# Optimization experiments

Measured on AMD Instinct MI355X. Metric: run time of the kernel, lower is better.

The kernel has to match this reference:

```python
import jax, jax.numpy as jnp
import numpy as np

P = 16           # patch size
D = 768          # embed / feature dim (= 3*P*P)
T = 8            # number of task vectors
H_META = 192     # MetaNet hidden (= D // 4)


def patchify(x):
    # x: [B, 3, H, W] -> [B, N, 3*P*P]
    B, C, H, W = x.shape
    x = x.reshape(B, C, H // P, P, W // P, P)
    x = x.transpose(0, 2, 4, 1, 3, 5)
    return x.reshape(B, (H // P) * (W // P), C * P * P)


def encode(W1, b1, W2, b2, x):
    # base functional encoder f(params, x): shared weights over the batch
    patches = patchify(x)                       # [B, N, D]
    h = jax.nn.relu(patches @ W1 + b1)          # [B, N, D]
    pooled = h.mean(axis=1)                     # [B, D]
    return pooled @ W2 + b2                     # [B, D]


def setup_inputs() -> dict:
    key = jax.random.key(0)
    ks = jax.random.split(key, 14)
    B = 64
    s = 0.02
    return {
        "x":   jax.random.normal(ks[0], (B, 3, 224, 224), jnp.float32),
        # base model params
        "W1":  jax.random.normal(ks[1], (D, D), jnp.float32) * s,
        "b1":  jax.random.normal(ks[2], (D,), jnp.float32) * s,
        "W2":  jax.random.normal(ks[3], (D, D), jnp.float32) * s,
        "b2":  jax.random.normal(ks[4], (D,), jnp.float32) * s,
        # task-vector deltas (stacked over T tasks)
        "dW1": jax.random.normal(ks[5], (T, D, D), jnp.float32) * s,
        "db1": jax.random.normal(ks[6], (T, D), jnp.float32) * s,
        "dW2": jax.random.normal(ks[7], (T, D, D), jnp.float32) * s,
        "db2": jax.random.normal(ks[8], (T, D), jnp.float32) * s,
        # MetaNet (Linear-ReLU-Linear); zero-init in the original, random here
        "mw1": jax.random.normal(ks[9], (D, H_META), jnp.float32) * s,
        "mb1": jax.random.normal(ks[10], (H_META,), jnp.float32) * s,
        "mw2": jax.random.normal(ks[11], (H_META, T), jnp.float32) * s,
        "mb2": jax.random.normal(ks[12], (T,), jnp.float32) * s,
    }


def reference(x, W1, b1, W2, b2, dW1, db1, dW2, db2, mw1, mb1, mw2, mb2):
    # 1) base features with frozen base model (torch.no_grad)
    base = jax.lax.stop_gradient(encode(W1, b1, W2, b2, x))       # [B, D]
    # 2) per-sample mixing coefficients via MetaNet
    coefs = jax.nn.relu(base @ mw1 + mb1) @ mw2 + mb2             # [B, T]
    # 3) per-sample mixed parameters: p + sum_t c[b,t] * dp[t]
    nW1 = W1 + jnp.einsum("bt,tij->bij", coefs, dW1)              # [B, D, D]
    nb1 = b1 + coefs @ db1                                        # [B, D]
    nW2 = W2 + jnp.einsum("bt,tij->bij", coefs, dW2)              # [B, D, D]
    nb2 = b2 + coefs @ db2                                        # [B, D]
    # 4) batched per-sample forward with the mixed weights
    patches = patchify(x)                                         # [B, N, D]
    h = jax.nn.relu(jnp.einsum("bnd,bde->bne", patches, nW1) + nb1[:, None, :])
    pooled = h.mean(axis=1)                                       # [B, D]
    out = jnp.einsum("bd,bde->be", pooled, nW2) + nb2             # [B, D]
    return out
```

## Files before the change

### kernel.cpp

```cpp
#include <hip/hip_runtime.h>
#include <hip/hip_bf16.h>


typedef __bf16 bf16x8 __attribute__((ext_vector_type(8)));
typedef float f32x4 __attribute__((ext_vector_type(4)));
typedef __hip_bfloat16 bf16;

struct alignas(16) BF8 { bf16 h[8]; };

constexpr int BATCH = 64;
constexpr int NP    = 196;
constexpr int NPAD  = 256;
constexpr int DIM   = 768;
constexpr int NT    = 8;
constexpr size_t MSZ = (size_t)DIM * DIM;

__device__ __forceinline__ void async_cp16(const void* g, void* l) {
  __builtin_amdgcn_global_load_lds(
      (const __attribute__((address_space(1))) uint32_t*)g,
      (__attribute__((address_space(3))) uint32_t*)l, 16, 0, 0);
}

constexpr int PREP_PATCH_BLOCKS = (BATCH * NPAD * (DIM / 4)) / 256;
constexpr int PREP_TRANS_BLOCKS = 24 * 24 * 18;

__global__ void k_prep(const float* __restrict__ x, bf16* __restrict__ A,
                       const float* __restrict__ W1, const float* __restrict__ dW1,
                       const float* __restrict__ W2, const float* __restrict__ dW2,
                       bf16* __restrict__ WT) {
  __shared__ float tile[32][33];
  int blk = blockIdx.x;
  int tid = threadIdx.x;
  if (blk < PREP_PATCH_BLOCKS) {
    int idx  = blk * 256 + tid;
    int col4 = idx % (DIM / 4);
    int row  = idx / (DIM / 4);
    int d = col4 * 4;
    int b = row >> 8;
    int n = row & 255;
    bf16 tmp[4];
    if (n < NP) {
      int hp = n / 14, wp = n % 14;
      int c  = d >> 8;
      int rr = d & 255;
      int i = rr >> 4, j = rr & 15;
      const float* src = x + ((((size_t)b * 3 + c) * 224 + hp * 16 + i) * 224 + wp * 16 + j);
      float4 f = *(const float4*)src;
      tmp[0] = __float2bfloat16(f.x);
      tmp[1] = __float2bfloat16(f.y);
      tmp[2] = __float2bfloat16(f.z);
      tmp[3] = __float2bfloat16(f.w);
    } else {
      tmp[0] = tmp[1] = tmp[2] = tmp[3] = __float2bfloat16(0.0f);
    }
    *(ushort4*)(A + (size_t)row * DIM + d) = *(ushort4*)tmp;
  } else {
    int tb  = blk - PREP_PATCH_BLOCKS;
    int mat = tb / 576;
    int rem = tb % 576;
    int n0 = (rem % 24) * 32;
    int k0 = (rem / 24) * 32;
    const float* src;
    if      (mat == 0) src = W1;
    else if (mat <= 8) src = dW1 + (size_t)(mat - 1) * MSZ;
    else if (mat == 9) src = W2;
    else               src = dW2 + (size_t)(mat - 10) * MSZ;
    int tx = tid & 31, ty = tid >> 5;
#pragma unroll
    for (int r = ty; r < 32; r += 8)
      tile[r][tx] = src[(size_t)(k0 + r) * DIM + n0 + tx];
    __syncthreads();
    bf16* dst = WT + (size_t)mat * MSZ;
#pragma unroll
    for (int r = ty; r < 32; r += 8)
      dst[(size_t)(n0 + r) * DIM + k0 + tx] = __float2bfloat16(tile[tx][r]);
  }
}


#define WAITVM(N) asm volatile("s_waitcnt vmcnt(" #N ")" ::: "memory")

template<int MIX>
__global__ __launch_bounds__(256, 3)
void k_gemm_pool(const bf16* __restrict__ A,
                 const bf16* __restrict__ WT,
                 const float* __restrict__ b1,
                 const float* __restrict__ db1,
                 const float* __restrict__ coefs,
                 float* __restrict__ pooled) {
  __shared__ uint4 AslU[3][896];
  __shared__ uint4 BslU[2][256];

  int b  = blockIdx.x;
  int n0 = blockIdx.y * 64;
  int tid = threadIdx.x;
  int wave = tid >> 6, lane = tid & 63;
  int quad = lane >> 4, l16 = lane & 15;

  float cr[NT];
  if (MIX) {
#pragma unroll
    for (int t = 0; t < NT; t++) cr[t] = coefs[b * NT + t];
  }

  const bf16* Ag = A + (size_t)b * NPAD * DIM;
  f32x4 acc[4][4] = {};

  int gbase = (wave < 2) ? wave * 256 : 512 + (wave - 2) * 192;
  int gcnt  = (wave < 2) ? 4 : 3;
  int aoff[4];
#pragma unroll
  for (int i = 0; i < 4; i++) {
    int s = gbase + i * 64 + lane;
    int p = s >> 3, u = (s & 7) ^ (p & 7);
    int r = 2 * p + (u >> 2), c = u & 3;
    aoff[i] = r * DIM + c * 8;
  }
  auto stage_a = [&](int buf, int kt) {
    const bf16* Ak = Ag + kt * 32;
#pragma unroll
    for (int i = 0; i < 4; i++) {
      if (i < gcnt)
        async_cp16(Ak + aoff[i], (void*)&AslU[buf][gbase + i * 64]);
    }
  };

  int bp = tid >> 3, bu = (tid & 7) ^ (bp & 7);
  int brow_st = 2 * bp + (bu >> 2), bcol_st = bu & 3;
  const bf16* Wrow = WT + (size_t)(n0 + brow_st) * DIM + bcol_st * 8;

  BF8 wreg[MIX ? 9 : 1];
  auto breg_load = [&](int kt) {
    const bf16* p0 = Wrow + kt * 32;
    wreg[0] = *(const BF8*)p0;
    if (MIX) {
#pragma unroll
      for (int t = 0; t < NT; t++)
        wreg[1 + t] = *(const BF8*)(p0 + (size_t)(1 + t) * MSZ);
    }
  };
  auto breg_write = [&](int buf) {
    if (MIX) {
      float m[8];
#pragma unroll
      for (int j = 0; j < 8; j++) m[j] = __bfloat162float(wreg[0].h[j]);
#pragma unroll
      for (int t = 0; t < NT; t++) {
        float cc = cr[t];
#pragma unroll
        for (int j = 0; j < 8; j++) m[j] += cc * __bfloat162float(wreg[1 + t].h[j]);
      }
      BF8 o;
#pragma unroll
      for (int j = 0; j < 8; j++) o.h[j] = __float2bfloat16(m[j]);
      BslU[buf][tid] = *(uint4*)&o;
    } else {
      BslU[buf][tid] = *(uint4*)&wreg[0];
    }
  };

  auto gslot = [&](int row, int kq) {
    return (size_t)((row >> 1) * 8 + ((4 * (row & 1) + kq) ^ ((row >> 1) & 7)));
  };

  stage_a(0, 0);
  stage_a(1, 1);
  breg_load(0);
  WAITVM(0);
  __builtin_amdgcn_sched_barrier(0);
  breg_write(0);
  asm volatile("s_waitcnt lgkmcnt(0)" ::: "memory");

  int bufA = 0, stgA = 2, bufB = 0;
  for (int kt = 0; kt < 24; kt++) {
    __builtin_amdgcn_s_barrier();
    if (kt < 23) breg_load(kt + 1);
    __builtin_amdgcn_sched_barrier(0);
    if (kt < 22) stage_a(stgA, kt + 2);
    __builtin_amdgcn_sched_barrier(0);
    const bf16* As = (const bf16*)AslU[bufA];
    const bf16* Bs = (const bf16*)BslU[bufB];
    bf16x8 bfr[4];
#pragma unroll
    for (int nf = 0; nf < 4; nf++) {
      int brow = nf * 16 + l16;
      bfr[nf] = *(const bf16x8*)(Bs + gslot(brow, quad) * 8);
    }
    __builtin_amdgcn_s_setprio(1);
#pragma unroll
    for (int mf = 0; mf < 4; mf++) {
      if (wave * 64 + mf * 16 < 224) {
        int arow = wave * 64 + mf * 16 + l16;
        bf16x8 af = *(const bf16x8*)(As + gslot(arow, quad) * 8);
#pragma unroll
        for (int nf = 0; nf < 4; nf++)
          acc[mf][nf] = __builtin_amdgcn_mfma_f32_16x16x32_bf16(af, bfr[nf], acc[mf][nf], 0, 0, 0);
      }
    }
    __builtin_amdgcn_s_setprio(0);
    if (kt < 22) {
      if (wave < 2) WAITVM(4); else WAITVM(3);
    } else if (kt < 23) {
      WAITVM(0);
    }
    __builtin_amdgcn_sched_barrier(0);
    if (kt < 23) {
      breg_write(bufB ^ 1);
      asm volatile("s_waitcnt lgkmcnt(0)" ::: "memory");
    }
    bufA = (bufA == 2) ? 0 : bufA + 1;
    stgA = (stgA == 2) ? 0 : stgA + 1;
    bufB ^= 1;
  }

  float* red = (float*)&BslU[0][0];
  int m0 = wave * 64;
  float colsum[4];
#pragma unroll
  for (int nf = 0; nf < 4; nf++) {
    int col = n0 + nf * 16 + l16;
    float bias = b1[col];
    if (MIX) {
#pragma unroll
      for (int t = 0; t < NT; t++) bias += cr[t] * db1[t * DIM + col];
    }
    float s = 0.0f;
#pragma unroll
    for (int mf = 0; mf < 4; mf++) {
      int rbase = m0 + mf * 16 + quad * 4;
#pragma unroll
      for (int r = 0; r < 4; r++) {
        if (rbase + r < NP) s += fmaxf(acc[mf][nf][r] + bias, 0.0f);
      }
    }
    s += __shfl_xor(s, 16, 64);
    s += __shfl_xor(s, 32, 64);
    colsum[nf] = s;
  }
  if (lane < 16) {
#pragma unroll
    for (int nf = 0; nf < 4; nf++) red[wave * 64 + nf * 16 + lane] = colsum[nf];
  }
  __syncthreads();
  if (tid < 64) {
    float s = red[tid] + red[64 + tid] + red[128 + tid] + red[192 + tid];
    pooled[(size_t)b * DIM + n0 + tid] = s * (1.0f / 196.0f);
  }
}

__global__ __launch_bounds__(256, 2)
void k_gemm2_ksplit(const float* __restrict__ Af,
                    const bf16* __restrict__ WT,
                    float* __restrict__ basep) {
  __shared__ uint4 AslU[64 * 8];
  __shared__ uint4 BslU[64 * 8];
  int n0  = blockIdx.x * 64;
  int kz  = blockIdx.y;
  int tid = threadIdx.x, wave = tid >> 6, lane = tid & 63;
  int quad = lane >> 4, l16 = lane & 15;
  f32x4 acc[4] = {};
  const bf16* Wm = WT + (size_t)9 * MSZ;
  for (int k0 = kz * 192; k0 < kz * 192 + 192; k0 += 64) {
#pragma unroll
    for (int i = 0; i < 2; i++) {
      int g = tid + i * 256;
      int r = g >> 3, c = g & 7;
      const float* src = Af + (size_t)r * DIM + k0 + c * 8;
      float4 xa = ((const float4*)src)[0];
      float4 xb = ((const float4*)src)[1];
      BF8 o;
      o.h[0] = __float2bfloat16(xa.x); o.h[1] = __float2bfloat16(xa.y);
      o.h[2] = __float2bfloat16(xa.z); o.h[3] = __float2bfloat16(xa.w);
      o.h[4] = __float2bfloat16(xb.x); o.h[5] = __float2bfloat16(xb.y);
      o.h[6] = __float2bfloat16(xb.z); o.h[7] = __float2bfloat16(xb.w);
      AslU[r * 8 + (c ^ (r & 7))] = *(uint4*)&o;
      BslU[r * 8 + (c ^ (r & 7))] = *(const uint4*)(Wm + (size_t)(n0 + r) * DIM + k0 + c * 8);
    }
    __syncthreads();
    const bf16* As = (const bf16*)AslU;
    const bf16* Bs = (const bf16*)BslU;
#pragma unroll
    for (int ks = 0; ks < 2; ks++) {
      int brow = wave * 16 + l16;
      bf16x8 bfr = *(const bf16x8*)(Bs + (size_t)(brow * 8 + ((ks * 4 + quad) ^ (brow & 7))) * 8);
#pragma unroll
      for (int mf = 0; mf < 4; mf++) {
        int arow = mf * 16 + l16;
        bf16x8 af = *(const bf16x8*)(As + (size_t)(arow * 8 + ((ks * 4 + quad) ^ (arow & 7))) * 8);
        acc[mf] = __builtin_amdgcn_mfma_f32_16x16x32_bf16(af, bfr, acc[mf], 0, 0, 0);
      }
    }
    __syncthreads();
  }
#pragma unroll
  for (int mf = 0; mf < 4; mf++) {
#pragma unroll
    for (int r = 0; r < 4; r++) {
      int row = mf * 16 + quad * 4 + r;
      int col = n0 + wave * 16 + l16;
      basep[((size_t)kz * 64 + row) * DIM + col] = acc[mf][r];
    }
  }
}

__global__ __launch_bounds__(256, 2)
void k_gemm2(const float* __restrict__ Af,
             const bf16* __restrict__ WT,
             int matbase,
             const float* __restrict__ bias,
             float* __restrict__ Y) {
  __shared__ uint4 AslU[64 * 8];
  __shared__ uint4 BslU[64 * 8];
  int n0  = blockIdx.x * 64;
  int mat = blockIdx.y;
  int tid = threadIdx.x, wave = tid >> 6, lane = tid & 63;
  int quad = lane >> 4, l16 = lane & 15;
  f32x4 acc[4] = {};
  const bf16* Wm = WT + (size_t)(matbase + mat) * MSZ;
  for (int k0 = 0; k0 < DIM; k0 += 64) {
#pragma unroll
    for (int i = 0; i < 2; i++) {
      int g = tid + i * 256;
      int r = g >> 3, c = g & 7;
      const float* src = Af + (size_t)r * DIM + k0 + c * 8;
      float4 xa = ((const float4*)src)[0];
      float4 xb = ((const float4*)src)[1];
      BF8 o;
      o.h[0] = __float2bfloat16(xa.x); o.h[1] = __float2bfloat16(xa.y);
      o.h[2] = __float2bfloat16(xa.z); o.h[3] = __float2bfloat16(xa.w);
      o.h[4] = __float2bfloat16(xb.x); o.h[5] = __float2bfloat16(xb.y);
      o.h[6] = __float2bfloat16(xb.z); o.h[7] = __float2bfloat16(xb.w);
      AslU[r * 8 + (c ^ (r & 7))] = *(uint4*)&o;
      BslU[r * 8 + (c ^ (r & 7))] = *(const uint4*)(Wm + (size_t)(n0 + r) * DIM + k0 + c * 8);
    }
    __syncthreads();
    const bf16* As = (const bf16*)AslU;
    const bf16* Bs = (const bf16*)BslU;
#pragma unroll
    for (int ks = 0; ks < 2; ks++) {
      int brow = wave * 16 + l16;
      bf16x8 bfr = *(const bf16x8*)(Bs + (size_t)(brow * 8 + ((ks * 4 + quad) ^ (brow & 7))) * 8);
#pragma unroll
      for (int mf = 0; mf < 4; mf++) {
        int arow = mf * 16 + l16;
        bf16x8 af = *(const bf16x8*)(As + (size_t)(arow * 8 + ((ks * 4 + quad) ^ (arow & 7))) * 8);
        acc[mf] = __builtin_amdgcn_mfma_f32_16x16x32_bf16(af, bfr, acc[mf], 0, 0, 0);
      }
    }
    __syncthreads();
  }
#pragma unroll
  for (int mf = 0; mf < 4; mf++) {
#pragma unroll
    for (int r = 0; r < 4; r++) {
      int row = mf * 16 + quad * 4 + r;
      int col = n0 + wave * 16 + l16;
      float v = acc[mf][r];
      if (bias) v += bias[col];
      Y[((size_t)mat * 64 + row) * DIM + col] = v;
    }
  }
}

__global__ void k_metanet(const float* __restrict__ basep,
                          const float* __restrict__ b2,
                          const float* __restrict__ mw1, const float* __restrict__ mb1,
                          const float* __restrict__ mw2, const float* __restrict__ mb2,
                          float* __restrict__ coefs) {
  __shared__ float bl[DIM];
  __shared__ float hl[192];
  int b = blockIdx.x, tid = threadIdx.x;
  const size_t ZS = (size_t)64 * DIM;
  for (int i = tid; i < DIM; i += 192) {
    size_t o = (size_t)b * DIM + i;
    bl[i] = basep[o] + basep[ZS + o] + basep[2 * ZS + o] + basep[3 * ZS + o] + b2[i];
  }
  __syncthreads();
  float s = mb1[tid];
  for (int k = 0; k < DIM; k++) s += bl[k] * mw1[(size_t)k * 192 + tid];
  hl[tid] = fmaxf(s, 0.0f);
  __syncthreads();
  if (tid < NT) {
    float c = mb2[tid];
    for (int j = 0; j < 192; j++) c += hl[j] * mw2[(size_t)j * NT + tid];
    coefs[b * NT + tid] = c;
  }
}

__global__ void k_combine(const float* __restrict__ Y,
                          const float* __restrict__ coefs,
                          const float* __restrict__ b2,
                          const float* __restrict__ db2,
                          float* __restrict__ out) {
  int idx = blockIdx.x * 256 + threadIdx.x;
  int b = idx / DIM, e = idx % DIM;
  float v = Y[(size_t)b * DIM + e] + b2[e];
#pragma unroll
  for (int t = 0; t < NT; t++) {
    float c = coefs[b * NT + t];
    v += c * (Y[((size_t)(1 + t) * 64 + b) * DIM + e] + db2[(size_t)t * DIM + e]);
  }
  out[idx] = v;
}

extern "C" void kernel_launch(void* const* d_in, const int* in_sizes, int n_in,
                              void* d_out, int out_size, void* d_ws, size_t ws_size,
                              hipStream_t stream) {
  const float* x   = (const float*)d_in[0];
  const float* W1  = (const float*)d_in[1];
  const float* b1  = (const float*)d_in[2];
  const float* W2  = (const float*)d_in[3];
  const float* b2  = (const float*)d_in[4];
  const float* dW1 = (const float*)d_in[5];
  const float* db1 = (const float*)d_in[6];
  const float* dW2 = (const float*)d_in[7];
  const float* db2 = (const float*)d_in[8];
  const float* mw1 = (const float*)d_in[9];
  const float* mb1 = (const float*)d_in[10];
  const float* mw2 = (const float*)d_in[11];
  const float* mb2 = (const float*)d_in[12];
  float* out = (float*)d_out;
  (void)in_sizes; (void)n_in; (void)out_size; (void)ws_size;

  char* ws = (char*)d_ws;
  bf16*  A_bf    = (bf16*) (ws);
  bf16*  WT      = (bf16*) (ws + 25165824);
  float* pooledA = (float*)(ws + 46399488);
  float* pooledB = (float*)(ws + 46596096);
  float* coefs   = (float*)(ws + 46792704);
  float* basep   = (float*)(ws + 46794752);
  float* Y       = (float*)(ws + 47581184);

  k_prep<<<dim3(PREP_PATCH_BLOCKS + PREP_TRANS_BLOCKS), 256, 0, stream>>>(
      x, A_bf, W1, dW1, W2, dW2, WT);
  k_gemm_pool<0><<<dim3(BATCH, DIM / 64), 256, 0, stream>>>(A_bf, WT, b1, db1, nullptr, pooledA);
  k_gemm2_ksplit<<<dim3(DIM / 64, 4), 256, 0, stream>>>(pooledA, WT, basep);
  k_metanet<<<dim3(BATCH), 192, 0, stream>>>(basep, b2, mw1, mb1, mw2, mb2, coefs);
  k_gemm_pool<1><<<dim3(BATCH, DIM / 64), 256, 0, stream>>>(A_bf, WT, b1, db1, coefs, pooledB);
  k_gemm2<<<dim3(DIM / 64, 9), 256, 0, stream>>>(pooledB, WT, 9, nullptr, Y);
  k_combine<<<dim3((BATCH * DIM) / 256), 256, 0, stream>>>(Y, coefs, b2, db2, out);
}
```

Baseline: 285.2 us.

## Fuse coefficient mixing into second GEMM with K-split and register-prefetched weights

Replaces the 9-matrix second-layer GEMM plus combine kernel with a K-split kernel where each block computes all 9 matrix products for its column tile. The coefficient-weighted sum is applied in the epilogue, so only 4 partial outputs are written instead of 9 full outputs. The pooled A tile is loaded once per K-slice and reused across all 9 weight matrices, with the next weight tile prefetched into registers and the LDS B buffer double-buffered. The cost is 144 accumulator registers per thread, which lowers occupancy, and a grid of only 48 blocks.

Result: no change. 289.5 us (+1.5%).

```diff
diff --git a/kernel.cpp b/kernel.cpp
--- a/kernel.cpp
+++ b/kernel.cpp
@@ -303,21 +303,56 @@
   }
 }
 
-__global__ __launch_bounds__(256, 2)
-void k_gemm2(const float* __restrict__ Af,
-             const bf16* __restrict__ WT,
-             int matbase,
-             const float* __restrict__ bias,
-             float* __restrict__ Y) {
+__global__ void k_metanet(const float* __restrict__ basep,
+                          const float* __restrict__ b2,
+                          const float* __restrict__ mw1, const float* __restrict__ mb1,
+                          const float* __restrict__ mw2, const float* __restrict__ mb2,
+                          float* __restrict__ coefs) {
+  __shared__ float bl[DIM];
+  __shared__ float hl[192];
+  int b = blockIdx.x, tid = threadIdx.x;
+  const size_t ZS = (size_t)64 * DIM;
+  for (int i = tid; i < DIM; i += 192) {
+    size_t o = (size_t)b * DIM + i;
+    bl[i] = basep[o] + basep[ZS + o] + basep[2 * ZS + o] + basep[3 * ZS + o] + b2[i];
+  }
+  __syncthreads();
+  float s = mb1[tid];
+  for (int k = 0; k < DIM; k++) s += bl[k] * mw1[(size_t)k * 192 + tid];
+  hl[tid] = fmaxf(s, 0.0f);
+  __syncthreads();
+  if (tid < NT) {
+    float c = mb2[tid];
+    for (int j = 0; j < 192; j++) c += hl[j] * mw2[(size_t)j * NT + tid];
+    coefs[b * NT + tid] = c;
+  }
+}
+
+__global__ __launch_bounds__(256)
+void k_gemm2c(const float* __restrict__ Af,
+              const bf16* __restrict__ WT,
+              const float* __restrict__ coefs,
+              float* __restrict__ Yp) {
   __shared__ uint4 AslU[64 * 8];
-  __shared__ uint4 BslU[64 * 8];
+  __shared__ uint4 BslU[2][64 * 8];
+  __shared__ float cl[64][8];
   int n0  = blockIdx.x * 64;
-  int mat = blockIdx.y;
+  int kz  = blockIdx.y;
   int tid = threadIdx.x, wave = tid >> 6, lane = tid & 63;
   int quad = lane >> 4, l16 = lane & 15;
-  f32x4 acc[4] = {};
-  const bf16* Wm = WT + (size_t)(matbase + mat) * MSZ;
-  for (int k0 = 0; k0 < DIM; k0 += 64) {
+
+  ((float*)cl)[tid]       = coefs[tid];
+  ((float*)cl)[256 + tid] = coefs[256 + tid];
+
+  int r0 = tid >> 3,         c0 = tid & 7;
+  int r1 = (tid + 256) >> 3, c1 = (tid + 256) & 7;
+  int bs0 = r0 * 8 + (c0 ^ (r0 & 7));
+  int bs1 = r1 * 8 + (c1 ^ (r1 & 7));
+
+  f32x4 acc[9][4] = {};
+
+  for (int kt = 0; kt < 3; kt++) {
+    int k0 = kz * 192 + kt * 64;
 #pragma unroll
     for (int i = 0; i < 2; i++) {
       int g = tid + i * 256;
@@ -331,75 +366,72 @@
       o.h[4] = __float2bfloat16(xb.x); o.h[5] = __float2bfloat16(xb.y);
       o.h[6] = __float2bfloat16(xb.z); o.h[7] = __float2bfloat16(xb.w);
       AslU[r * 8 + (c ^ (r & 7))] = *(uint4*)&o;
-      BslU[r * 8 + (c ^ (r & 7))] = *(const uint4*)(Wm + (size_t)(n0 + r) * DIM + k0 + c * 8);
-    }
+    }
+    const bf16* W0 = WT + (size_t)9 * MSZ + k0;
+    uint4 rcur0 = *(const uint4*)(W0 + (size_t)(n0 + r0) * DIM + c0 * 8);
+    uint4 rcur1 = *(const uint4*)(W0 + (size_t)(n0 + r1) * DIM + c1 * 8);
     __syncthreads();
     const bf16* As = (const bf16*)AslU;
-    const bf16* Bs = (const bf16*)BslU;
-#pragma unroll
-    for (int ks = 0; ks < 2; ks++) {
-      int brow = wave * 16 + l16;
-      bf16x8 bfr = *(const bf16x8*)(Bs + (size_t)(brow * 8 + ((ks * 4 + quad) ^ (brow & 7))) * 8);
+    bf16x8 af[2][4];
+#pragma unroll
+    for (int ks = 0; ks < 2; ks++)
 #pragma unroll
       for (int mf = 0; mf < 4; mf++) {
         int arow = mf * 16 + l16;
-        bf16x8 af = *(const bf16x8*)(As + (size_t)(arow * 8 + ((ks * 4 + quad) ^ (arow & 7))) * 8);
-        acc[mf] = __builtin_amdgcn_mfma_f32_16x16x32_bf16(af, bfr, acc[mf], 0, 0, 0);
-      }
+        af[ks][mf] = *(const bf16x8*)(As + (size_t)(arow * 8 + ((ks * 4 + quad) ^ (arow & 7))) * 8);
+      }
+#pragma unroll
+    for (int m = 0; m < 9; m++) {
+      uint4 rnxt0, rnxt1;
+      if (m < 8) {
+        const bf16* Wn = WT + (size_t)(10 + m) * MSZ + k0;
+        rnxt0 = *(const uint4*)(Wn + (size_t)(n0 + r0) * DIM + c0 * 8);
+        rnxt1 = *(const uint4*)(Wn + (size_t)(n0 + r1) * DIM + c1 * 8);
+      }
+      BslU[m & 1][bs0] = rcur0;
+      BslU[m & 1][bs1] = rcur1;
+      __syncthreads();
+      const bf16* Bs = (const bf16*)&BslU[m & 1][0];
+#pragma unroll
+      for (int ks = 0; ks < 2; ks++) {
+        int brow = wave * 16 + l16;
+        bf16x8 bfr = *(const bf16x8*)(Bs + (size_t)(brow * 8 + ((ks * 4 + quad) ^ (brow & 7))) * 8);
+#pragma unroll
+        for (int mf = 0; mf < 4; mf++)
+          acc[m][mf] = __builtin_amdgcn_mfma_f32_16x16x32_bf16(af[ks][mf], bfr, acc[m][mf], 0, 0, 0);
+      }
+      rcur0 = rnxt0;
+      rcur1 = rnxt1;
     }
     __syncthreads();
   }
+
 #pragma unroll
   for (int mf = 0; mf < 4; mf++) {
 #pragma unroll
     for (int r = 0; r < 4; r++) {
       int row = mf * 16 + quad * 4 + r;
       int col = n0 + wave * 16 + l16;
-      float v = acc[mf][r];
-      if (bias) v += bias[col];
-      Y[((size_t)mat * 64 + row) * DIM + col] = v;
-    }
-  }
-}
-
-__global__ void k_metanet(const float* __restrict__ basep,
-                          const float* __restrict__ b2,
-                          const float* __restrict__ mw1, const float* __restrict__ mb1,
-                          const float* __restrict__ mw2, const float* __restrict__ mb2,
-                          float* __restrict__ coefs) {
-  __shared__ float bl[DIM];
-  __shared__ float hl[192];
-  int b = blockIdx.x, tid = threadIdx.x;
-  const size_t ZS = (size_t)64 * DIM;
-  for (int i = tid; i < DIM; i += 192) {
-    size_t o = (size_t)b * DIM + i;
-    bl[i] = basep[o] + basep[ZS + o] + basep[2 * ZS + o] + basep[3 * ZS + o] + b2[i];
-  }
-  __syncthreads();
-  float s = mb1[tid];
-  for (int k = 0; k < DIM; k++) s += bl[k] * mw1[(size_t)k * 192 + tid];
-  hl[tid] = fmaxf(s, 0.0f);
-  __syncthreads();
-  if (tid < NT) {
-    float c = mb2[tid];
-    for (int j = 0; j < 192; j++) c += hl[j] * mw2[(size_t)j * NT + tid];
-    coefs[b * NT + tid] = c;
-  }
-}
-
-__global__ void k_combine(const float* __restrict__ Y,
-                          const float* __restrict__ coefs,
-                          const float* __restrict__ b2,
-                          const float* __restrict__ db2,
-                          float* __restrict__ out) {
+      float v = acc[0][mf][r];
+#pragma unroll
+      for (int t = 0; t < NT; t++) v += cl[row][t] * acc[1 + t][mf][r];
+      Yp[((size_t)kz * 64 + row) * DIM + col] = v;
+    }
+  }
+}
+
+__global__ void k_sum4(const float* __restrict__ Yp,
+                       const float* __restrict__ coefs,
+                       const float* __restrict__ b2,
+                       const float* __restrict__ db2,
+                       float* __restrict__ out) {
   int idx = blockIdx.x * 256 + threadIdx.x;
   int b = idx / DIM, e = idx % DIM;
-  float v = Y[(size_t)b * DIM + e] + b2[e];
-#pragma unroll
-  for (int t = 0; t < NT; t++) {
-    float c = coefs[b * NT + t];
-    v += c * (Y[((size_t)(1 + t) * 64 + b) * DIM + e] + db2[(size_t)t * DIM + e]);
-  }
+  const size_t ZS = (size_t)64 * DIM;
+  float v = Yp[idx] + Yp[ZS + idx] + Yp[2 * ZS + idx] + Yp[3 * ZS + idx] + b2[e];
+#pragma unroll
+  for (int t = 0; t < NT; t++)
+    v += coefs[b * NT + t] * db2[(size_t)t * DIM + e];
   out[idx] = v;
 }
 
@@ -429,7 +461,7 @@
   float* pooledB = (float*)(ws + 46596096);
   float* coefs   = (float*)(ws + 46792704);
   float* basep   = (float*)(ws + 46794752);
-  float* Y       = (float*)(ws + 47581184);
+  float* Yp      = (float*)(ws + 47581184);
 
   k_prep<<<dim3(PREP_PATCH_BLOCKS + PREP_TRANS_BLOCKS), 256, 0, stream>>>(
       x, A_bf, W1, dW1, W2, dW2, WT);
@@ -437,6 +469,6 @@
   k_gemm2_ksplit<<<dim3(DIM / 64, 4), 256, 0, stream>>>(pooledA, WT, basep);
   k_metanet<<<dim3(BATCH), 192, 0, stream>>>(basep, b2, mw1, mb1, mw2, mb2, coefs);
   k_gemm_pool<1><<<dim3(BATCH, DIM / 64), 256, 0, stream>>>(A_bf, WT, b1, db1, coefs, pooledB);
-  k_gemm2<<<dim3(DIM / 64, 9), 256, 0, stream>>>(pooledB, WT, 9, nullptr, Y);
-  k_combine<<<dim3((BATCH * DIM) / 256), 256, 0, stream>>>(Y, coefs, b2, db2, out);
-}
+  k_gemm2c<<<dim3(DIM / 64, 4), 256, 0, stream>>>(pooledB, WT, coefs, Yp);
+  k_sum4<<<dim3((BATCH * DIM) / 256), 256, 0, stream>>>(Yp, coefs, b2, db2, out);
+}
```

## Add dedicated wide-tile base GEMM-pool kernel with async-staged weights

Applied to the files above, without the earlier changes.

Replaces the non-mixing instantiation of the templated GEMM+pool kernel with a dedicated 512-thread kernel that computes a 224x192 output tile per block, staging both patches and base weights into LDS via async global-to-LDS copies in a triple buffer. Larger N tiles cut redundant reloads of the patch matrix (4 blocks per sample instead of 12) and raise MFMA work per LDS fetch. The mixing kernel becomes a non-template kernel and gemm2 loses its unused bias/matbase parameters. In exchange, the new kernel uses more registers (21 accumulators) and more LDS per block, which may limit occupancy.

Result: no change. 286.4 us (+0.4%).

```diff
diff --git a/kernel.cpp b/kernel.cpp
--- a/kernel.cpp
+++ b/kernel.cpp
@@ -20,6 +20,8 @@
       (const __attribute__((address_space(1))) uint32_t*)g,
       (__attribute__((address_space(3))) uint32_t*)l, 16, 0, 0);
 }
+
+#define WAITVM(N) asm volatile("s_waitcnt vmcnt(" #N ")" ::: "memory")
 
 constexpr int PREP_PATCH_BLOCKS = (BATCH * NPAD * (DIM / 4)) / 256;
 constexpr int PREP_TRANS_BLOCKS = 24 * 24 * 18;
@@ -77,17 +79,122 @@
   }
 }
 
-
-#define WAITVM(N) asm volatile("s_waitcnt vmcnt(" #N ")" ::: "memory")
-
-template<int MIX>
+__global__ __launch_bounds__(512, 2)
+void k_gemm_poolA(const bf16* __restrict__ A,
+                  const bf16* __restrict__ WT,
+                  const float* __restrict__ b1,
+                  float* __restrict__ pooled) {
+  __shared__ uint4 AslU[3][896];
+  __shared__ uint4 BslU[3][768];
+  __shared__ float red[8][48];
+
+  int b  = blockIdx.x;
+  int n0 = blockIdx.y * 192;
+  int tid = threadIdx.x;
+  int w = tid >> 6, lane = tid & 63;
+  int quad = lane >> 4, l16 = lane & 15;
+  int wm = w & 1, wn = w >> 1;
+
+  const bf16* Ag = A + (size_t)b * NPAD * DIM;
+  const bf16* Bg = WT + (size_t)n0 * DIM;
+
+  f32x4 acc[7][3] = {};
+
+  int off0, off1;
+  {
+    int s = w * 64 + lane;
+    int p = s >> 3, u = (s & 7) ^ (p & 7);
+    off0 = (2 * p + (u >> 2)) * DIM + (u & 3) * 8;
+    int s1 = 512 + w * 64 + lane;
+    int p1 = s1 >> 3, u1 = (s1 & 7) ^ (p1 & 7);
+    off1 = (2 * p1 + (u1 >> 2)) * DIM + (u1 & 3) * 8;
+  }
+  auto stage_ab = [&](int buf, int kt) {
+    const bf16* Ak = Ag + kt * 32;
+    const bf16* Bk = Bg + kt * 32;
+    async_cp16(Ak + off0, (void*)&AslU[buf][w * 64]);
+    if (w < 6) async_cp16(Ak + off1, (void*)&AslU[buf][512 + w * 64]);
+    async_cp16(Bk + off0, (void*)&BslU[buf][w * 64]);
+    if (w < 4) async_cp16(Bk + off1, (void*)&BslU[buf][512 + w * 64]);
+  };
+  auto gslot = [&](int row, int kq) {
+    return (size_t)((row >> 1) * 8 + ((4 * (row & 1) + kq) ^ ((row >> 1) & 7)));
+  };
+
+  stage_ab(0, 0);
+  stage_ab(1, 1);
+  WAITVM(0);
+  __builtin_amdgcn_sched_barrier(0);
+
+  int bufA = 0, stgA = 2;
+  for (int kt = 0; kt < 24; kt++) {
+    __builtin_amdgcn_s_barrier();
+    if (kt < 22) stage_ab(stgA, kt + 2);
+    __builtin_amdgcn_sched_barrier(0);
+    const bf16* As = (const bf16*)AslU[bufA];
+    const bf16* Bs = (const bf16*)BslU[bufA];
+    bf16x8 bfr[3];
+#pragma unroll
+    for (int nf = 0; nf < 3; nf++) {
+      int brow = wn * 48 + nf * 16 + l16;
+      bfr[nf] = *(const bf16x8*)(Bs + gslot(brow, quad) * 8);
+    }
+    __builtin_amdgcn_s_setprio(1);
+#pragma unroll
+    for (int mf = 0; mf < 7; mf++) {
+      int arow = wm * 112 + mf * 16 + l16;
+      bf16x8 af = *(const bf16x8*)(As + gslot(arow, quad) * 8);
+#pragma unroll
+      for (int nf = 0; nf < 3; nf++)
+        acc[mf][nf] = __builtin_amdgcn_mfma_f32_16x16x32_bf16(af, bfr[nf], acc[mf][nf], 0, 0, 0);
+    }
+    __builtin_amdgcn_s_setprio(0);
+    if (kt < 22) {
+      if (w < 4) WAITVM(4); else if (w < 6) WAITVM(3); else WAITVM(2);
+    } else if (kt < 23) {
+      WAITVM(0);
+    }
+    __builtin_amdgcn_sched_barrier(0);
+    bufA = (bufA == 2) ? 0 : bufA + 1;
+    stgA = (stgA == 2) ? 0 : stgA + 1;
+  }
+
+  float colsum[3];
+#pragma unroll
+  for (int nf = 0; nf < 3; nf++) {
+    float bias = b1[n0 + wn * 48 + nf * 16 + l16];
+    float s = 0.0f;
+#pragma unroll
+    for (int mf = 0; mf < 7; mf++) {
+      int rbase = wm * 112 + mf * 16 + quad * 4;
+#pragma unroll
+      for (int r = 0; r < 4; r++) {
+        if (rbase + r < NP) s += fmaxf(acc[mf][nf][r] + bias, 0.0f);
+      }
+    }
+    s += __shfl_xor(s, 16, 64);
+    s += __shfl_xor(s, 32, 64);
+    colsum[nf] = s;
+  }
+  if (lane < 16) {
+#pragma unroll
+    for (int nf = 0; nf < 3; nf++) red[w][nf * 16 + lane] = colsum[nf];
+  }
+  __syncthreads();
+  if (tid < 192) {
+    int wn2 = tid / 48, off = tid % 48;
+    float s = red[2 * wn2][off] + red[2 * wn2 + 1][off];
+    pooled[(size_t)b * DIM + n0 + tid] = s * (1.0f / 196.0f);
+  }
+}
+
 __global__ __launch_bounds__(256, 3)
-void k_gemm_pool(const bf16* __restrict__ A,
-                 const bf16* __restrict__ WT,
-                 const float* __restrict__ b1,
-                 const float* __restrict__ db1,
-                 const float* __restrict__ coefs,
-                 float* __restrict__ pooled) {
+void k_gemm_pool_mix(const bf16* __restrict__ A,
+                     const bf16* __restrict__ WT,
+                     const float* __restrict__ b1,
+                     const float* __restrict__ db1,
+                     const float* __restrict__ coefs,
+                     float* __restrict__ pooled) {
   __shared__ uint4 AslU[3][896];
   __shared__ uint4 BslU[2][256];
 
@@ -98,10 +205,8 @@
   int quad = lane >> 4, l16 = lane & 15;
 
   float cr[NT];
-  if (MIX) {
-#pragma unroll
-    for (int t = 0; t < NT; t++) cr[t] = coefs[b * NT + t];
-  }
+#pragma unroll
+  for (int t = 0; t < NT; t++) cr[t] = coefs[b * NT + t];
 
   const bf16* Ag = A + (size_t)b * NPAD * DIM;
   f32x4 acc[4][4] = {};
@@ -129,34 +234,28 @@
   int brow_st = 2 * bp + (bu >> 2), bcol_st = bu & 3;
   const bf16* Wrow = WT + (size_t)(n0 + brow_st) * DIM + bcol_st * 8;
 
-  BF8 wreg[MIX ? 9 : 1];
+  BF8 wreg[9];
   auto breg_load = [&](int kt) {
     const bf16* p0 = Wrow + kt * 32;
     wreg[0] = *(const BF8*)p0;
-    if (MIX) {
-#pragma unroll
-      for (int t = 0; t < NT; t++)
-        wreg[1 + t] = *(const BF8*)(p0 + (size_t)(1 + t) * MSZ);
-    }
+#pragma unroll
+    for (int t = 0; t < NT; t++)
+      wreg[1 + t] = *(const BF8*)(p0 + (size_t)(1 + t) * MSZ);
   };
   auto breg_write = [&](int buf) {
-    if (MIX) {
-      float m[8];
-#pragma unroll
-      for (int j = 0; j < 8; j++) m[j] = __bfloat162float(wreg[0].h[j]);
-#pragma unroll
-      for (int t = 0; t < NT; t++) {
-        float cc = cr[t];
-#pragma unroll
-        for (int j = 0; j < 8; j++) m[j] += cc * __bfloat162float(wreg[1 + t].h[j]);
-      }
-      BF8 o;
-#pragma unroll
-      for (int j = 0; j < 8; j++) o.h[j] = __float2bfloat16(m[j]);
-      BslU[buf][tid] = *(uint4*)&o;
-    } else {
-      BslU[buf][tid] = *(uint4*)&wreg[0];
-    }
+    float m[8];
+#pragma unroll
+    for (int j = 0; j < 8; j++) m[j] = __bfloat162float(wreg[0].h[j]);
+#pragma unroll
+    for (int t = 0; t < NT; t++) {
+      float cc = cr[t];
+#pragma unroll
+      for (int j = 0; j < 8; j++) m[j] += cc * __bfloat162float(wreg[1 + t].h[j]);
+    }
+    BF8 o;
+#pragma unroll
+    for (int j = 0; j < 8; j++) o.h[j] = __float2bfloat16(m[j]);
+    BslU[buf][tid] = *(uint4*)&o;
   };
 
   auto gslot = [&](int row, int kq) {
@@ -220,10 +319,8 @@
   for (int nf = 0; nf < 4; nf++) {
     int col = n0 + nf * 16 + l16;
     float bias = b1[col];
-    if (MIX) {
-#pragma unroll
-      for (int t = 0; t < NT; t++) bias += cr[t] * db1[t * DIM + col];
-    }
+#pragma unroll
+    for (int t = 0; t < NT; t++) bias += cr[t] * db1[t * DIM + col];
     float s = 0.0f;
 #pragma unroll
     for (int mf = 0; mf < 4; mf++) {
@@ -303,11 +400,34 @@
   }
 }
 
+__global__ void k_metanet(const float* __restrict__ basep,
+                          const float* __restrict__ b2,
+                          const float* __restrict__ mw1, const float* __restrict__ mb1,
+                          const float* __restrict__ mw2, const float* __restrict__ mb2,
+                          float* __restrict__ coefs) {
+  __shared__ float bl[DIM];
+  __shared__ float hl[192];
+  int b = blockIdx.x, tid = threadIdx.x;
+  const size_t ZS = (size_t)64 * DIM;
+  for (int i = tid; i < DIM; i += 192) {
+    size_t o = (size_t)b * DIM + i;
+    bl[i] = basep[o] + basep[ZS + o] + basep[2 * ZS + o] + basep[3 * ZS + o] + b2[i];
+  }
+  __syncthreads();
+  float s = mb1[tid];
+  for (int k = 0; k < DIM; k++) s += bl[k] * mw1[(size_t)k * 192 + tid];
+  hl[tid] = fmaxf(s, 0.0f);
+  __syncthreads();
+  if (tid < NT) {
+    float c = mb2[tid];
+    for (int j = 0; j < 192; j++) c += hl[j] * mw2[(size_t)j * NT + tid];
+    coefs[b * NT + tid] = c;
+  }
+}
+
 __global__ __launch_bounds__(256, 2)
 void k_gemm2(const float* __restrict__ Af,
              const bf16* __restrict__ WT,
-             int matbase,
-             const float* __restrict__ bias,
              float* __restrict__ Y) {
   __shared__ uint4 AslU[64 * 8];
   __shared__ uint4 BslU[64 * 8];
@@ -316,7 +436,7 @@
   int tid = threadIdx.x, wave = tid >> 6, lane = tid & 63;
   int quad = lane >> 4, l16 = lane & 15;
   f32x4 acc[4] = {};
-  const bf16* Wm = WT + (size_t)(matbase + mat) * MSZ;
+  const bf16* Wm = WT + (size_t)(9 + mat) * MSZ;
   for (int k0 = 0; k0 < DIM; k0 += 64) {
 #pragma unroll
     for (int i = 0; i < 2; i++) {
@@ -355,35 +475,8 @@
     for (int r = 0; r < 4; r++) {
       int row = mf * 16 + quad * 4 + r;
       int col = n0 + wave * 16 + l16;
-      float v = acc[mf][r];
-      if (bias) v += bias[col];
-      Y[((size_t)mat * 64 + row) * DIM + col] = v;
-    }
-  }
-}
-
-__global__ void k_metanet(const float* __restrict__ basep,
-                          const float* __restrict__ b2,
-                          const float* __restrict__ mw1, const float* __restrict__ mb1,
-                          const float* __restrict__ mw2, const float* __restrict__ mb2,
-                          float* __restrict__ coefs) {
-  __shared__ float bl[DIM];
-  __shared__ float hl[192];
-  int b = blockIdx.x, tid = threadIdx.x;
-  const size_t ZS = (size_t)64 * DIM;
-  for (int i = tid; i < DIM; i += 192) {
-    size_t o = (size_t)b * DIM + i;
-    bl[i] = basep[o] + basep[ZS + o] + basep[2 * ZS + o] + basep[3 * ZS + o] + b2[i];
-  }
-  __syncthreads();
-  float s = mb1[tid];
-  for (int k = 0; k < DIM; k++) s += bl[k] * mw1[(size_t)k * 192 + tid];
-  hl[tid] = fmaxf(s, 0.0f);
-  __syncthreads();
-  if (tid < NT) {
-    float c = mb2[tid];
-    for (int j = 0; j < 192; j++) c += hl[j] * mw2[(size_t)j * NT + tid];
-    coefs[b * NT + tid] = c;
+      Y[((size_t)mat * 64 + row) * DIM + col] = acc[mf][r];
+    }
   }
 }
 
@@ -433,10 +526,10 @@
 
   k_prep<<<dim3(PREP_PATCH_BLOCKS + PREP_TRANS_BLOCKS), 256, 0, stream>>>(
       x, A_bf, W1, dW1, W2, dW2, WT);
-  k_gemm_pool<0><<<dim3(BATCH, DIM / 64), 256, 0, stream>>>(A_bf, WT, b1, db1, nullptr, pooledA);
+  k_gemm_poolA<<<dim3(BATCH, DIM / 192), 512, 0, stream>>>(A_bf, WT, b1, pooledA);
   k_gemm2_ksplit<<<dim3(DIM / 64, 4), 256, 0, stream>>>(pooledA, WT, basep);
   k_metanet<<<dim3(BATCH), 192, 0, stream>>>(basep, b2, mw1, mb1, mw2, mb2, coefs);
-  k_gemm_pool<1><<<dim3(BATCH, DIM / 64), 256, 0, stream>>>(A_bf, WT, b1, db1, coefs, pooledB);
-  k_gemm2<<<dim3(DIM / 64, 9), 256, 0, stream>>>(pooledB, WT, 9, nullptr, Y);
+  k_gemm_pool_mix<<<dim3(BATCH, DIM / 64), 256, 0, stream>>>(A_bf, WT, b1, db1, coefs, pooledB);
+  k_gemm2<<<dim3(DIM / 64, 9), 256, 0, stream>>>(pooledB, WT, Y);
   k_combine<<<dim3((BATCH * DIM) / 256), 256, 0, stream>>>(Y, coefs, b2, db2, out);
 }
```
